# Optimization experiments

Measured on AMD Instinct MI355X. Metric: run time of the kernel, lower is better.

## Reference

```python
import jax, jax.numpy as jnp
import numpy as np

N_DRUG = 100000
N_PROT = 100000
N_EDGE = 800000
DIM = 128


def _graph_conv(feat_src, esrc, edst, n_src, n_dst, W, b):
    """dgl GraphConv with norm='both': msg = h_src * outdeg^-1/2, sum over in-edges,
    scale by indeg^-1/2, then linear. Degrees clamped to >= 1."""
    ones = jnp.ones(esrc.shape[0], dtype=feat_src.dtype)
    deg_out = jnp.clip(jax.ops.segment_sum(ones, esrc, num_segments=n_src), 1.0)
    deg_in = jnp.clip(jax.ops.segment_sum(ones, edst, num_segments=n_dst), 1.0)
    h = feat_src * jax.lax.rsqrt(deg_out)[:, None]          # [n_src, d]
    agg = jax.ops.segment_sum(h[esrc], edst, num_segments=n_dst)  # [n_dst, d]
    agg = agg * jax.lax.rsqrt(deg_in)[:, None]
    return agg @ W + b


def _hetero_layer(hd, hp, ddi_src, ddi_dst, pdi_src, pdi_dst, ppi_src, ppi_dst, W, b):
    # relation order: 0=DDI (drug->drug), 1=PDI (protein->drug), 2=PPI (protein->protein)
    d_ddi = _graph_conv(hd, ddi_src, ddi_dst, N_DRUG, N_DRUG, W[0], b[0])
    d_pdi = _graph_conv(hp, pdi_src, pdi_dst, N_PROT, N_DRUG, W[1], b[1])
    p_ppi = _graph_conv(hp, ppi_src, ppi_dst, N_PROT, N_PROT, W[2], b[2])
    return d_ddi + d_pdi, p_ppi  # HeteroGraphConv aggregate='sum' per dst type


def setup_inputs() -> dict:
    key = jax.random.key(0)
    ks = jax.random.split(key, 16)
    s = 1.0 / np.sqrt(DIM)
    return {
        "drug_feats": jax.random.normal(ks[0], (N_DRUG, DIM), jnp.float32),
        "protein_feats": jax.random.normal(ks[1], (N_PROT, DIM), jnp.float32),
        "ddi_src": jax.random.randint(ks[2], (N_EDGE,), 0, N_DRUG),
        "ddi_dst": jax.random.randint(ks[3], (N_EDGE,), 0, N_DRUG),
        "pdi_src": jax.random.randint(ks[4], (N_EDGE,), 0, N_PROT),
        "pdi_dst": jax.random.randint(ks[5], (N_EDGE,), 0, N_DRUG),
        "ppi_src": jax.random.randint(ks[6], (N_EDGE,), 0, N_PROT),
        "ppi_dst": jax.random.randint(ks[7], (N_EDGE,), 0, N_PROT),
        "W1": jax.random.normal(ks[8], (3, DIM, DIM), jnp.float32) * s,
        "b1": jnp.zeros((3, DIM), jnp.float32),
        "W2": jax.random.normal(ks[9], (3, DIM, DIM), jnp.float32) * s,
        "b2": jnp.zeros((3, DIM), jnp.float32),
        "W3": jax.random.normal(ks[10], (3, DIM, DIM), jnp.float32) * s,
        "b3": jnp.zeros((3, DIM), jnp.float32),
    }


def reference(drug_feats, protein_feats, ddi_src, ddi_dst, pdi_src, pdi_dst,
              ppi_src, ppi_dst, W1, b1, W2, b2, W3, b3):
    e = (ddi_src, ddi_dst, pdi_src, pdi_dst, ppi_src, ppi_dst)
    hd, hp = _hetero_layer(drug_feats, protein_feats, *e, W1, b1)
    hd, hp = jax.nn.relu(hd), jax.nn.relu(hp)
    hd, hp = _hetero_layer(hd, hp, *e, W2, b2)
    hd, hp = jax.nn.relu(hd), jax.nn.relu(hp)
    hd, hp = _hetero_layer(hd, hp, *e, W3, b3)
    return hd, hp
```

## Files before the change

### kernel.cpp

```cpp
#include <hip/hip_runtime.h>
#include <hip/hip_bf16.h>
#include <stdint.h>

#define NN 100000
#define NE 800000
#define SCAN_CHUNK 2048
#define NBLK 49

#define NPART 8
#define PART_SZ ((NN + NPART - 1) / NPART)
#define CSR_EPT 4
#define CSR_CHUNK (256 * CSR_EPT)
#define CSR_CB ((NE + CSR_CHUNK - 1) / CSR_CHUNK)

#define KSPLIT 4
#define SEGSZ (NE / KSPLIT)
#define HBINS 12500

typedef __bf16 bf16x8 __attribute__((ext_vector_type(8)));
using float4v = __attribute__((ext_vector_type(4))) float;
typedef int intv4 __attribute__((ext_vector_type(4)));

__device__ __forceinline__ float bf2f(unsigned short h) {
    unsigned int u = ((unsigned int)h) << 16;
    return __builtin_bit_cast(float, u);
}
__device__ __forceinline__ float bf_lo(unsigned int u) {
    return __builtin_bit_cast(float, u << 16);
}
__device__ __forceinline__ float bf_hi(unsigned int u) {
    return __builtin_bit_cast(float, u & 0xffff0000u);
}
__device__ __forceinline__ unsigned short f2bf(float x) {
    unsigned int u = __builtin_bit_cast(unsigned int, x);
    u += 0x7fffu + ((u >> 16) & 1u);
    return (unsigned short)(u >> 16);
}

__global__ void detect_fmt(const unsigned short* __restrict__ feat, int* __restrict__ flag) {
    __shared__ int cnt;
    if (threadIdx.x == 0) cnt = 0;
    __syncthreads();
    unsigned int u = feat[threadIdx.x];
    int e = (u >> 7) & 0xFF;
    if (e >= 90 && e <= 143) atomicAdd(&cnt, 1);
    __syncthreads();
    if (threadIdx.x == 0) {
        flag[0] = (cnt >= 160) ? 0 : 1;
        flag[1] = 0;
    }
}

__global__ __launch_bounds__(256) void convert_feats(const void* __restrict__ drug,
                                                     const void* __restrict__ prot,
                                                     unsigned short* __restrict__ hd,
                                                     unsigned short* __restrict__ hp,
                                                     const int* __restrict__ fmtp) {
    int fmt = fmtp[0];
    int i = (blockIdx.x * 256 + threadIdx.x) * 4;
    const int n1 = NN * 128;
    if (i >= 2 * n1) return;
    const void* src = (i < n1) ? drug : prot;
    unsigned short* dst = (i < n1) ? hd : hp;
    int j = (i < n1) ? i : i - n1;
    if (fmt) {
        float4 v = *(const float4*)((const float*)src + j);
        uint2 o;
        o.x = (unsigned int)f2bf(v.x) | ((unsigned int)f2bf(v.y) << 16);
        o.y = (unsigned int)f2bf(v.z) | ((unsigned int)f2bf(v.w) << 16);
        *(uint2*)(dst + j) = o;
    } else {
        *(uint2*)(dst + j) = *(const uint2*)((const unsigned short*)src + j);
    }
}

__global__ __launch_bounds__(256) void deg_hist(const int* __restrict__ s0, const int* __restrict__ d0,
                                                const int* __restrict__ s1, const int* __restrict__ d1,
                                                const int* __restrict__ s2, const int* __restrict__ d2,
                                                int* __restrict__ deg_part) {
    __shared__ unsigned int cnt[HBINS];
    int h = blockIdx.y;
    const int* a;
    switch (h) {
        case 0: a = s0; break;
        case 1: a = s1; break;
        case 2: a = s2; break;
        case 3: a = d0; break;
        case 4: a = d1; break;
        default: a = d2; break;
    }
    int part = blockIdx.x & (NPART - 1);
    int seg = blockIdx.x >> 3;
    int lo = part * HBINS;
    for (int j = threadIdx.x; j < HBINS; j += 256) cnt[j] = 0;
    __syncthreads();
    int base = seg * SEGSZ;
    int end = base + SEGSZ;
    for (int i = base + threadIdx.x * 4; i + 4 <= end; i += 1024) {
        intv4 v = *(const intv4*)(a + i);
#pragma unroll
        for (int k = 0; k < 4; k++) {
            int b = v[k] - lo;
            if ((unsigned)b < (unsigned)HBINS) atomicAdd(&cnt[b], 1u);
        }
    }
    __syncthreads();
    int* outp = deg_part + (size_t)seg * 6 * NN + h * NN + lo;
    for (int j = threadIdx.x; j < HBINS; j += 256) outp[j] = (int)cnt[j];
}

__global__ __launch_bounds__(256) void merge_deg_rs(const int* __restrict__ deg_part,
                                                    int* __restrict__ deg_all,
                                                    float* __restrict__ rs_all) {
    int i = (blockIdx.x * 256 + threadIdx.x) * 4;
    if (i >= 6 * NN) return;
    intv4 acc = *(const intv4*)(deg_part + i);
#pragma unroll
    for (int s = 1; s < KSPLIT; s++) {
        intv4 v = *(const intv4*)(deg_part + (size_t)s * 6 * NN + i);
        acc += v;
    }
    *(intv4*)(deg_all + i) = acc;
    float4v r;
#pragma unroll
    for (int k = 0; k < 4; k++) {
        int d = acc[k];
        if (d < 1) d = 1;
        r[k] = rsqrtf((float)d);
    }
    *(float4v*)(rs_all + i) = r;
}

__global__ __launch_bounds__(256) void scan_partial(const int* __restrict__ deg,
                                                    int* __restrict__ bsums) {
    int rel = blockIdx.y, blk = blockIdx.x;
    const int* d = deg + rel * NN;
    int base = blk * SCAN_CHUNK + threadIdx.x * 8;
    int s = 0;
#pragma unroll
    for (int i = 0; i < 8; i++) {
        int idx = base + i;
        if (idx < NN) s += d[idx];
    }
    __shared__ int wsum[4];
#pragma unroll
    for (int off = 32; off; off >>= 1) s += __shfl_down(s, off);
    if ((threadIdx.x & 63) == 0) wsum[threadIdx.x >> 6] = s;
    __syncthreads();
    if (threadIdx.x == 0) bsums[rel * NBLK + blk] = wsum[0] + wsum[1] + wsum[2] + wsum[3];
}

__global__ void scan_bsums(int* bsums) {
    int r = threadIdx.x;
    if (r < 3) {
        int run = 0;
        for (int i = 0; i < NBLK; i++) {
            int t = bsums[r * NBLK + i];
            bsums[r * NBLK + i] = run;
            run += t;
        }
    }
}

__global__ __launch_bounds__(256) void scan_final(const int* __restrict__ deg,
                                                  const int* __restrict__ bsums,
                                                  int* __restrict__ offs,
                                                  int* __restrict__ cursor) {
    int rel = blockIdx.y, blk = blockIdx.x;
    const int* d = deg + rel * NN;
    int* o = offs + rel * NN;
    int* c = cursor + rel * NN;
    int base = blk * SCAN_CHUNK + threadIdx.x * 8;
    int v[8];
    int s = 0;
#pragma unroll
    for (int i = 0; i < 8; i++) {
        int idx = base + i;
        v[i] = (idx < NN) ? d[idx] : 0;
        s += v[i];
    }
    int lane = threadIdx.x & 63, wid = threadIdx.x >> 6;
    int x = s;
#pragma unroll
    for (int off = 1; off < 64; off <<= 1) {
        int t = __shfl_up(x, off);
        if (lane >= off) x += t;
    }
    __shared__ int wsum[4];
    if (lane == 63) wsum[wid] = x;
    __syncthreads();
    int woff = bsums[rel * NBLK + blk];
    for (int i = 0; i < wid; i++) woff += wsum[i];
    int run = woff + x - s;
#pragma unroll
    for (int i = 0; i < 8; i++) {
        int idx = base + i;
        if (idx < NN) {
            o[idx] = run;
            c[idx] = run;
            run += v[i];
        }
    }
}

__global__ __launch_bounds__(256) void csr_fill3p(const int* __restrict__ s0, const int* __restrict__ d0,
                                                  const int* __restrict__ s1, const int* __restrict__ d1,
                                                  const int* __restrict__ s2, const int* __restrict__ d2,
                                                  int* __restrict__ cursor_all, int* __restrict__ csr_all) {
    int rel = blockIdx.y;
    const int* s = (rel == 0) ? s0 : ((rel == 1) ? s1 : s2);
    const int* d = (rel == 0) ? d0 : ((rel == 1) ? d1 : d2);
    int part = blockIdx.x & (NPART - 1);
    int chunk = blockIdx.x >> 3;
    int lo = part * PART_SZ;
    int hi = lo + PART_SZ;
    int* cur = cursor_all + rel * NN;
    int* csr = csr_all + (size_t)rel * NE;
    int base = chunk * CSR_CHUNK + threadIdx.x * CSR_EPT;
    if (base + CSR_EPT <= NE) {
        intv4 dv = __builtin_nontemporal_load((const intv4*)(d + base));
        intv4 sv = __builtin_nontemporal_load((const intv4*)(s + base));
#pragma unroll
        for (int i = 0; i < 4; i++) {
            int dd = dv[i];
            if (dd >= lo && dd < hi) {
                int pos = atomicAdd(&cur[dd], 1);
                csr[pos] = sv[i];
            }
        }
    } else {
#pragma unroll
        for (int i = 0; i < CSR_EPT; i++) {
            int idx = base + i;
            if (idx < NE) {
                int dd = d[idx];
                if (dd >= lo && dd < hi) {
                    int pos = atomicAdd(&cur[dd], 1);
                    csr[pos] = s[idx];
                }
            }
        }
    }
}

__global__ __launch_bounds__(256) void swizzle_w3(const void* __restrict__ W0,
                                                  const void* __restrict__ W1,
                                                  const void* __restrict__ W2,
                                                  int o0, int o1,
                                                  unsigned short* __restrict__ out, int lstride,
                                                  const int* __restrict__ fmtp, int ksteps) {
    int l = blockIdx.y;
    const void* W = (l == 0) ? W0 : ((l == 1) ? W1 : W2);
    int fmt = fmtp[0];
    int idx = blockIdx.x * 256 + threadIdx.x;
    int total = ksteps * 8 * 64 * 8;
    if (idx >= total) return;
    int j = idx & 7, lane = (idx >> 3) & 63, nt = (idx >> 9) & 7, ks = idx >> 12;
    int k = ks * 32 + (lane >> 4) * 8 + j;
    int n = nt * 16 + (lane & 15);
    int e = (k < 128) ? (o0 + k * 128 + n) : (o1 + (k - 128) * 128 + n);
    out[l * lstride + idx] = fmt ? f2bf(((const float*)W)[e]) : ((const unsigned short*)W)[e];
}

__global__ void bias_prep3(const void* __restrict__ b0, const void* __restrict__ b1,
                           const void* __restrict__ b2, float* __restrict__ bd,
                           float* __restrict__ bp, const int* __restrict__ fmtp) {
    int l = blockIdx.x;
    const void* b = (l == 0) ? b0 : ((l == 1) ? b1 : b2);
    int fmt = fmtp[0];
    int n = threadIdx.x;
    float v0, v1, v2;
    if (fmt) {
        const float* bf = (const float*)b;
        v0 = bf[n]; v1 = bf[128 + n]; v2 = bf[256 + n];
    } else {
        const unsigned short* bh = (const unsigned short*)b;
        v0 = bf2f(bh[n]); v1 = bf2f(bh[128 + n]); v2 = bf2f(bh[256 + n]);
    }
    bd[l * 128 + n] = v0 + v1;
    bp[l * 128 + n] = v2;
}

__device__ __forceinline__ void acc8(float* acc, uint4 v, float w) {
    acc[0] = fmaf(bf_lo(v.x), w, acc[0]);
    acc[1] = fmaf(bf_hi(v.x), w, acc[1]);
    acc[2] = fmaf(bf_lo(v.y), w, acc[2]);
    acc[3] = fmaf(bf_hi(v.y), w, acc[3]);
    acc[4] = fmaf(bf_lo(v.z), w, acc[4]);
    acc[5] = fmaf(bf_hi(v.z), w, acc[5]);
    acc[6] = fmaf(bf_lo(v.w), w, acc[6]);
    acc[7] = fmaf(bf_hi(v.w), w, acc[7]);
}

__global__ __launch_bounds__(256) void aggregate3(const unsigned short* __restrict__ hd,
                                                  const unsigned short* __restrict__ hp,
                                                  const float* __restrict__ rs_all,
                                                  const int* __restrict__ offs_all,
                                                  const int* __restrict__ deg_in_all,
                                                  const int* __restrict__ csr_all,
                                                  unsigned short* __restrict__ aggD,
                                                  unsigned short* __restrict__ aggP) {
    int rel = blockIdx.y;
    int g = blockIdx.x * 256 + threadIdx.x;
    int dst = g >> 4;
    int lane = g & 15;
    if (dst >= NN) return;
    const unsigned short* h = (rel == 0) ? hd : hp;
    const float* rs_out = rs_all + rel * NN;
    const float* rs_in = rs_all + (3 + rel) * NN;
    const int* cp = csr_all + (size_t)rel * NE + offs_all[rel * NN + dst];
    int cnt = deg_in_all[rel * NN + dst];
    unsigned short* out;
    int ostride, ocol;
    if (rel == 0)      { out = aggD; ostride = 256; ocol = 0; }
    else if (rel == 1) { out = aggD; ostride = 256; ocol = 128; }
    else               { out = aggP; ostride = 128; ocol = 0; }

    float acc[8] = {0.f, 0.f, 0.f, 0.f, 0.f, 0.f, 0.f, 0.f};
    int e = 0;
    for (; e + 4 <= cnt; e += 4) {
        int i0 = cp[e], i1 = cp[e + 1], i2 = cp[e + 2], i3 = cp[e + 3];
        float w0 = rs_out[i0], w1 = rs_out[i1], w2 = rs_out[i2], w3 = rs_out[i3];
        uint4 v0 = *(const uint4*)(h + (size_t)i0 * 128 + lane * 8);
        uint4 v1 = *(const uint4*)(h + (size_t)i1 * 128 + lane * 8);
        uint4 v2 = *(const uint4*)(h + (size_t)i2 * 128 + lane * 8);
        uint4 v3 = *(const uint4*)(h + (size_t)i3 * 128 + lane * 8);
        acc8(acc, v0, w0);
        acc8(acc, v1, w1);
        acc8(acc, v2, w2);
        acc8(acc, v3, w3);
    }
    for (; e < cnt; e++) {
        int i0 = cp[e];
        float w0 = rs_out[i0];
        uint4 v0 = *(const uint4*)(h + (size_t)i0 * 128 + lane * 8);
        acc8(acc, v0, w0);
    }
    float sc = rs_in[dst];
    uint4 o;
    o.x = (unsigned int)f2bf(acc[0] * sc) | ((unsigned int)f2bf(acc[1] * sc) << 16);
    o.y = (unsigned int)f2bf(acc[2] * sc) | ((unsigned int)f2bf(acc[3] * sc) << 16);
    o.z = (unsigned int)f2bf(acc[4] * sc) | ((unsigned int)f2bf(acc[5] * sc) << 16);
    o.w = (unsigned int)f2bf(acc[6] * sc) | ((unsigned int)f2bf(acc[7] * sc) << 16);
    *(uint4*)(out + (size_t)dst * ostride + ocol + lane * 8) = o;
}

__global__ __launch_bounds__(256) void gemm2(const unsigned short* __restrict__ A0,
                                             const unsigned short* __restrict__ B0,
                                             const float* __restrict__ bias0,
                                             void* __restrict__ out0, size_t ob0, int lda0, int nch0,
                                             const unsigned short* __restrict__ A1,
                                             const unsigned short* __restrict__ B1,
                                             const float* __restrict__ bias1,
                                             void* __restrict__ out1, size_t ob1, int lda1, int nch1,
                                             int relu, const int* __restrict__ ofmt) {
    __shared__ unsigned short bs[4 * 8 * 64 * 8];
    int y = blockIdx.y;
    const unsigned short* A = y ? A1 : A0;
    const unsigned short* Bf = y ? B1 : B0;
    const float* bias = y ? bias1 : bias0;
    void* outv = y ? out1 : out0;
    size_t obase = y ? ob1 : ob0;
    int lda = y ? lda1 : lda0;
    int nch = y ? nch1 : nch0;
    int fmt = ofmt[0];

    int lid = threadIdx.x & 63, wid = threadIdx.x >> 6;
    int m0 = blockIdx.x * 64 + wid * 16;
    int ra = m0 + (lid & 15);
    if (ra > NN - 1) ra = NN - 1;
    int koff = (lid >> 4) * 8;
    float4v acc[8];
#pragma unroll
    for (int nt = 0; nt < 8; nt++) acc[nt] = (float4v){0.f, 0.f, 0.f, 0.f};
    const unsigned short* arow = A + (size_t)ra * lda + koff;

    for (int c = 0; c < nch; c++) {
        if (c) __syncthreads();
        const uint4* gsrc = (const uint4*)(Bf + c * 16384);
        uint4* ldst = (uint4*)bs;
#pragma unroll
        for (int i = 0; i < 8; i++) ldst[threadIdx.x + i * 256] = gsrc[threadIdx.x + i * 256];
        __syncthreads();
#pragma unroll
        for (int ks = 0; ks < 4; ks++) {
            bf16x8 a = *(const bf16x8*)(arow + (c * 4 + ks) * 32);
            const bf16x8* bp = (const bf16x8*)bs + ks * 8 * 64 + lid;
#pragma unroll
            for (int nt = 0; nt < 8; nt++) {
                bf16x8 b = bp[nt * 64];
                acc[nt] = __builtin_amdgcn_mfma_f32_16x16x32_bf16(a, b, acc[nt], 0, 0, 0);
            }
        }
    }
    int crow = m0 + (lid >> 4) * 4;
    int ccol = lid & 15;
#pragma unroll
    for (int nt = 0; nt < 8; nt++) {
        float bb = bias[nt * 16 + ccol];
#pragma unroll
        for (int r = 0; r < 4; r++) {
            int row = crow + r;
            if (row < NN) {
                float yv = acc[nt][r] + bb;
                if (relu) yv = fmaxf(yv, 0.f);
                size_t idx = obase + (size_t)row * 128 + nt * 16 + ccol;
                if (fmt) ((float*)outv)[idx] = yv;
                else ((unsigned short*)outv)[idx] = f2bf(yv);
            }
        }
    }
}

__global__ __launch_bounds__(256) void copy_final(const void* __restrict__ src,
                                                  void* __restrict__ dst,
                                                  const int* __restrict__ fmtp, int n) {
    int fmt = fmtp[0];
    int i = (blockIdx.x * 256 + threadIdx.x) * 4;
    if (i < n) {
        if (fmt) *(float4*)((float*)dst + i) = *(const float4*)((const float*)src + i);
        else *(uint2*)((unsigned short*)dst + i) = *(const uint2*)((const unsigned short*)src + i);
    }
}

extern "C" void kernel_launch(void* const* d_in, const int* in_sizes, int n_in,
                              void* d_out, int out_size, void* d_ws, size_t ws_size,
                              hipStream_t stream) {
    (void)in_sizes; (void)n_in; (void)out_size;
    const void* drug = d_in[0];
    const void* prot = d_in[1];
    const int* ddi_src = (const int*)d_in[2];
    const int* ddi_dst = (const int*)d_in[3];
    const int* pdi_src = (const int*)d_in[4];
    const int* pdi_dst = (const int*)d_in[5];
    const int* ppi_src = (const int*)d_in[6];
    const int* ppi_dst = (const int*)d_in[7];
    const void* Wl[3] = {d_in[8], d_in[10], d_in[12]};
    const void* bl[3] = {d_in[9], d_in[11], d_in[13]};

    char* p = (char*)d_ws;
    auto alloc = [&](size_t bytes) -> char* {
        char* r = p;
        p += (bytes + 255) & ~(size_t)255;
        return r;
    };
    int*   flag       = (int*)alloc(256);
    int*   deg_all    = (int*)alloc(6 * NN * 4);
    float* rs_all     = (float*)alloc(6 * NN * 4);
    int*   offs_all   = (int*)alloc(3 * NN * 4);
    int*   cursor_all = (int*)alloc(3 * NN * 4);
    int*   csr_all    = (int*)alloc(3 * NE * 4);
    int*   bsums      = (int*)alloc(3 * NBLK * 4);
    char*  hbuf       = alloc((size_t)NN * 128 * 4);
    unsigned short* hd_b = (unsigned short*)hbuf;
    unsigned short* hp_b = (unsigned short*)hbuf + (size_t)NN * 128;
    unsigned short* aggP = (unsigned short*)alloc((size_t)NN * 128 * 2);
    unsigned short* Wd_f = (unsigned short*)alloc(3 * 8 * 8 * 64 * 8 * 2);
    unsigned short* Wp_f = (unsigned short*)alloc(3 * 4 * 8 * 64 * 8 * 2);
    float* bd = (float*)alloc(3 * 128 * 4);
    float* bp = (float*)alloc(3 * 128 * 4);
    size_t needed = (size_t)(p - (char*)d_ws);
    if (needed > ws_size) return;

    int* deg_part = csr_all;

    const int* FMT = flag;
    const int* BF  = flag + 1;

    unsigned short* aggD = (unsigned short*)d_out;

    detect_fmt<<<1, 256, 0, stream>>>((const unsigned short*)drug, flag);

    deg_hist<<<dim3(NPART * KSPLIT, 6), 256, 0, stream>>>(ddi_src, ddi_dst, pdi_src, pdi_dst,
                                                          ppi_src, ppi_dst, deg_part);
    merge_deg_rs<<<(6 * NN / 4 + 255) / 256, 256, 0, stream>>>(deg_part, deg_all, rs_all);
    scan_partial<<<dim3(NBLK, 3), 256, 0, stream>>>(deg_all + 3 * NN, bsums);
    scan_bsums<<<1, 64, 0, stream>>>(bsums);
    scan_final<<<dim3(NBLK, 3), 256, 0, stream>>>(deg_all + 3 * NN, bsums, offs_all, cursor_all);
    csr_fill3p<<<dim3(CSR_CB * NPART, 3), 256, 0, stream>>>(ddi_src, ddi_dst, pdi_src, pdi_dst,
                                                            ppi_src, ppi_dst, cursor_all, csr_all);

    swizzle_w3<<<dim3((8 * 8 * 64 * 8 + 255) / 256, 3), 256, 0, stream>>>(
        Wl[0], Wl[1], Wl[2], 0, 16384, Wd_f, 32768, FMT, 8);
    swizzle_w3<<<dim3((4 * 8 * 64 * 8 + 255) / 256, 3), 256, 0, stream>>>(
        Wl[0], Wl[1], Wl[2], 32768, 0, Wp_f, 16384, FMT, 4);
    bias_prep3<<<3, 128, 0, stream>>>(bl[0], bl[1], bl[2], bd, bp, FMT);

    convert_feats<<<(2 * NN * 128 / 4 + 255) / 256, 256, 0, stream>>>(drug, prot, hd_b, hp_b, FMT);

    const int AGB = (NN * 16 + 255) / 256;
    const int GGB = (NN + 63) / 64;
    for (int l = 0; l < 3; l++) {
        aggregate3<<<dim3(AGB, 3), 256, 0, stream>>>(hd_b, hp_b, rs_all, offs_all,
                                                     deg_all + 3 * NN, csr_all, aggD, aggP);
        if (l < 2) {
            gemm2<<<dim3(GGB, 2), 256, 0, stream>>>(
                aggD, Wd_f + l * 32768, bd + l * 128, hd_b, 0, 256, 2,
                aggP, Wp_f + l * 16384, bp + l * 128, hp_b, 0, 128, 1,
                1, BF);
        } else {
            gemm2<<<dim3(GGB, 1), 256, 0, stream>>>(
                aggD, Wd_f + l * 32768, bd + l * 128, hbuf, 0, 256, 2,
                aggD, Wd_f + l * 32768, bd + l * 128, hbuf, 0, 256, 2,
                0, FMT);
            gemm2<<<dim3(GGB, 1), 256, 0, stream>>>(
                aggP, Wp_f + l * 16384, bp + l * 128, d_out, (size_t)NN * 128, 128, 1,
                aggP, Wp_f + l * 16384, bp + l * 128, d_out, (size_t)NN * 128, 128, 1,
                0, FMT);
            copy_final<<<(NN * 128 / 4 + 255) / 256, 256, 0, stream>>>(hbuf, d_out, FMT, NN * 128);
        }
    }
}
```

Baseline: 853.3 us.

## Build CSR with per-segment LDS cursors instead of global atomics

CSR fill now uses per-(segment,partition) start offsets computed from per-segment degree histograms, so each block keeps its cursors in shared memory and does LDS atomics rather than global atomics on a cursor array. Degree partials are stored as 16-bit counts with KSPLIT raised to 16, and the buffers are aliased onto the feature and aggregation scratch. This adds a seg_start kernel and larger partial histograms, and it gives fewer blocks per relation in the fill. Each block also scans its whole segment for its partition.

Result: faster. 729.5 us (-14.5%).

```diff
diff --git a/kernel.cpp b/kernel.cpp
--- a/kernel.cpp
+++ b/kernel.cpp
@@ -9,17 +9,14 @@
 
 #define NPART 8
 #define PART_SZ ((NN + NPART - 1) / NPART)
-#define CSR_EPT 4
-#define CSR_CHUNK (256 * CSR_EPT)
-#define CSR_CB ((NE + CSR_CHUNK - 1) / CSR_CHUNK)
-
-#define KSPLIT 4
+#define KSPLIT 16
 #define SEGSZ (NE / KSPLIT)
-#define HBINS 12500
+#define HBINS PART_SZ
 
 typedef __bf16 bf16x8 __attribute__((ext_vector_type(8)));
 using float4v = __attribute__((ext_vector_type(4))) float;
 typedef int intv4 __attribute__((ext_vector_type(4)));
+typedef unsigned short ushortv4 __attribute__((ext_vector_type(4)));
 
 __device__ __forceinline__ float bf2f(unsigned short h) {
     unsigned int u = ((unsigned int)h) << 16;
@@ -77,7 +74,7 @@
 __global__ __launch_bounds__(256) void deg_hist(const int* __restrict__ s0, const int* __restrict__ d0,
                                                 const int* __restrict__ s1, const int* __restrict__ d1,
                                                 const int* __restrict__ s2, const int* __restrict__ d2,
-                                                int* __restrict__ deg_part) {
+                                                unsigned short* __restrict__ deg_part) {
     __shared__ unsigned int cnt[HBINS];
     int h = blockIdx.y;
     const int* a;
@@ -105,21 +102,22 @@
         }
     }
     __syncthreads();
-    int* outp = deg_part + (size_t)seg * 6 * NN + h * NN + lo;
-    for (int j = threadIdx.x; j < HBINS; j += 256) outp[j] = (int)cnt[j];
-}
-
-__global__ __launch_bounds__(256) void merge_deg_rs(const int* __restrict__ deg_part,
+    unsigned short* outp = deg_part + (size_t)seg * 6 * NN + (size_t)h * NN + lo;
+    for (int j = threadIdx.x; j < HBINS; j += 256) outp[j] = (unsigned short)cnt[j];
+}
+
+__global__ __launch_bounds__(256) void merge_deg_rs(const unsigned short* __restrict__ deg_part,
                                                     int* __restrict__ deg_all,
                                                     float* __restrict__ rs_all) {
     int i = (blockIdx.x * 256 + threadIdx.x) * 4;
     if (i >= 6 * NN) return;
-    intv4 acc = *(const intv4*)(deg_part + i);
-#pragma unroll
-    for (int s = 1; s < KSPLIT; s++) {
-        intv4 v = *(const intv4*)(deg_part + (size_t)s * 6 * NN + i);
-        acc += v;
-    }
+    int a0 = 0, a1 = 0, a2 = 0, a3 = 0;
+#pragma unroll
+    for (int s = 0; s < KSPLIT; s++) {
+        ushortv4 v = *(const ushortv4*)(deg_part + (size_t)s * 6 * NN + i);
+        a0 += v[0]; a1 += v[1]; a2 += v[2]; a3 += v[3];
+    }
+    intv4 acc; acc[0] = a0; acc[1] = a1; acc[2] = a2; acc[3] = a3;
     *(intv4*)(deg_all + i) = acc;
     float4v r;
 #pragma unroll
@@ -164,12 +162,10 @@
 
 __global__ __launch_bounds__(256) void scan_final(const int* __restrict__ deg,
                                                   const int* __restrict__ bsums,
-                                                  int* __restrict__ offs,
-                                                  int* __restrict__ cursor) {
+                                                  int* __restrict__ offs) {
     int rel = blockIdx.y, blk = blockIdx.x;
     const int* d = deg + rel * NN;
     int* o = offs + rel * NN;
-    int* c = cursor + rel * NN;
     int base = blk * SCAN_CHUNK + threadIdx.x * 8;
     int v[8];
     int s = 0;
@@ -197,47 +193,52 @@
         int idx = base + i;
         if (idx < NN) {
             o[idx] = run;
-            c[idx] = run;
             run += v[i];
         }
     }
 }
 
-__global__ __launch_bounds__(256) void csr_fill3p(const int* __restrict__ s0, const int* __restrict__ d0,
+__global__ __launch_bounds__(256) void seg_start_k(const unsigned short* __restrict__ deg_part,
+                                                   const int* __restrict__ offs_all,
+                                                   int* __restrict__ seg_start) {
+    int i = blockIdx.x * 256 + threadIdx.x;
+    if (i >= 3 * NN) return;
+    int rel = i / NN, node = i - rel * NN;
+    int run = offs_all[i];
+#pragma unroll
+    for (int s = 0; s < KSPLIT; s++) {
+        seg_start[((size_t)s * 3 + rel) * NN + node] = run;
+        run += deg_part[((size_t)s * 6 + 3 + rel) * NN + node];
+    }
+}
+
+__global__ __launch_bounds__(256) void csr_fill3s(const int* __restrict__ s0, const int* __restrict__ d0,
                                                   const int* __restrict__ s1, const int* __restrict__ d1,
                                                   const int* __restrict__ s2, const int* __restrict__ d2,
-                                                  int* __restrict__ cursor_all, int* __restrict__ csr_all) {
+                                                  const int* __restrict__ seg_start,
+                                                  int* __restrict__ csr_all) {
+    __shared__ int cur[PART_SZ];
     int rel = blockIdx.y;
     const int* s = (rel == 0) ? s0 : ((rel == 1) ? s1 : s2);
     const int* d = (rel == 0) ? d0 : ((rel == 1) ? d1 : d2);
     int part = blockIdx.x & (NPART - 1);
-    int chunk = blockIdx.x >> 3;
+    int seg = blockIdx.x >> 3;
     int lo = part * PART_SZ;
-    int hi = lo + PART_SZ;
-    int* cur = cursor_all + rel * NN;
+    const int* ss = seg_start + ((size_t)seg * 3 + rel) * NN + lo;
+    for (int j = threadIdx.x; j < PART_SZ; j += 256) cur[j] = ss[j];
+    __syncthreads();
     int* csr = csr_all + (size_t)rel * NE;
-    int base = chunk * CSR_CHUNK + threadIdx.x * CSR_EPT;
-    if (base + CSR_EPT <= NE) {
-        intv4 dv = __builtin_nontemporal_load((const intv4*)(d + base));
-        intv4 sv = __builtin_nontemporal_load((const intv4*)(s + base));
-#pragma unroll
-        for (int i = 0; i < 4; i++) {
-            int dd = dv[i];
-            if (dd >= lo && dd < hi) {
-                int pos = atomicAdd(&cur[dd], 1);
-                csr[pos] = sv[i];
-            }
-        }
-    } else {
-#pragma unroll
-        for (int i = 0; i < CSR_EPT; i++) {
-            int idx = base + i;
-            if (idx < NE) {
-                int dd = d[idx];
-                if (dd >= lo && dd < hi) {
-                    int pos = atomicAdd(&cur[dd], 1);
-                    csr[pos] = s[idx];
-                }
+    int base = seg * SEGSZ;
+    int end = base + SEGSZ;
+    for (int i = base + threadIdx.x * 4; i + 4 <= end; i += 1024) {
+        intv4 dv = *(const intv4*)(d + i);
+        intv4 sv = *(const intv4*)(s + i);
+#pragma unroll
+        for (int k = 0; k < 4; k++) {
+            int b = dv[k] - lo;
+            if ((unsigned)b < (unsigned)PART_SZ) {
+                int pos = atomicAdd(&cur[b], 1);
+                csr[pos] = sv[k];
             }
         }
     }
@@ -448,7 +449,6 @@
     int*   deg_all    = (int*)alloc(6 * NN * 4);
     float* rs_all     = (float*)alloc(6 * NN * 4);
     int*   offs_all   = (int*)alloc(3 * NN * 4);
-    int*   cursor_all = (int*)alloc(3 * NN * 4);
     int*   csr_all    = (int*)alloc(3 * NE * 4);
     int*   bsums      = (int*)alloc(3 * NBLK * 4);
     char*  hbuf       = alloc((size_t)NN * 128 * 4);
@@ -462,7 +462,8 @@
     size_t needed = (size_t)(p - (char*)d_ws);
     if (needed > ws_size) return;
 
-    int* deg_part = csr_all;
+    unsigned short* deg_part = (unsigned short*)hbuf;
+    int* seg_start = (int*)aggP;
 
     const int* FMT = flag;
     const int* BF  = flag + 1;
@@ -476,9 +477,10 @@
     merge_deg_rs<<<(6 * NN / 4 + 255) / 256, 256, 0, stream>>>(deg_part, deg_all, rs_all);
     scan_partial<<<dim3(NBLK, 3), 256, 0, stream>>>(deg_all + 3 * NN, bsums);
     scan_bsums<<<1, 64, 0, stream>>>(bsums);
-    scan_final<<<dim3(NBLK, 3), 256, 0, stream>>>(deg_all + 3 * NN, bsums, offs_all, cursor_all);
-    csr_fill3p<<<dim3(CSR_CB * NPART, 3), 256, 0, stream>>>(ddi_src, ddi_dst, pdi_src, pdi_dst,
-                                                            ppi_src, ppi_dst, cursor_all, csr_all);
+    scan_final<<<dim3(NBLK, 3), 256, 0, stream>>>(deg_all + 3 * NN, bsums, offs_all);
+    seg_start_k<<<(3 * NN + 255) / 256, 256, 0, stream>>>(deg_part, offs_all, seg_start);
+    csr_fill3s<<<dim3(NPART * KSPLIT, 3), 256, 0, stream>>>(ddi_src, ddi_dst, pdi_src, pdi_dst,
+                                                            ppi_src, ppi_dst, seg_start, csr_all);
 
     swizzle_w3<<<dim3((8 * 8 * 64 * 8 + 255) / 256, 3), 256, 0, stream>>>(
         Wl[0], Wl[1], Wl[2], 0, 16384, Wd_f, 32768, FMT, 8);
```
